# Kernel tuning notes

Measured on AMD Instinct MI355X. Metric: run time of the kernel, lower is better.

Reference implementation:

```python
import jax, jax.numpy as jnp
import numpy as np

B, T, N_EMBD, HEAD_SIZE = 4, 4096, 32, 32


def setup_inputs() -> dict:
    key = jax.random.key(0)
    k1, k2, k3, k4 = jax.random.split(key, 4)
    x = jax.random.normal(k1, (B, T, N_EMBD), dtype=jnp.float32)
    Wq = jax.random.normal(k2, (HEAD_SIZE, N_EMBD), dtype=jnp.float32) * (N_EMBD ** -0.5)
    Wk = jax.random.normal(k3, (HEAD_SIZE, N_EMBD), dtype=jnp.float32) * (N_EMBD ** -0.5)
    Wv = jax.random.normal(k4, (HEAD_SIZE, N_EMBD), dtype=jnp.float32) * (N_EMBD ** -0.5)
    return {"x": x, "Wq": Wq, "Wk": Wk, "Wv": Wv}


def reference(x, Wq, Wk, Wv):
    # Linear(bias=False): y = x @ W.T  -> [B, T, head_size]
    q = jnp.einsum('btn,hn->bth', x, Wq)
    k = jnp.einsum('btn,hn->bth', x, Wk)
    v = jnp.einsum('btn,hn->bth', x, Wv)
    scale = q.shape[-1] ** -0.5
    # [B, T, T] attention scores
    wei = jnp.einsum('bth,bsh->bts', q, k) * scale
    # Faithful to source: tril the scores, then mask entries equal to 0
    tril = jnp.tril(wei)
    wei = jax.nn.softmax(jnp.where(tril == 0, -jnp.inf, tril), axis=-1)
    return jnp.einsum('bts,bsh->bth', wei, v)
```

## Files before the change

### kernel.cpp

```cpp
#include <hip/hip_runtime.h>
#include <cmath>

#define BB 4
#define TT 4096
#define NE 32
#define HS 32

#define IPB 2176
#define MAXSP 16
#define SLOT 288
#define FNEG (-1.0e30f)
#define BIAS 6.0f

typedef unsigned int uint32;
typedef __fp16 half2v __attribute__((ext_vector_type(2)));
typedef __fp16 half4v __attribute__((ext_vector_type(4)));
typedef __fp16 half8v __attribute__((ext_vector_type(8)));
typedef float f32x4 __attribute__((ext_vector_type(4)));

__device__ __forceinline__ half2v u2h(uint32 u) {
    union { uint32 u; half2v h; } x; x.u = u; return x.h;
}

#if __has_builtin(__builtin_amdgcn_cvt_pkrtz)
__device__ __forceinline__ half2v pkf16(float a, float b) {
    return __builtin_amdgcn_cvt_pkrtz(a, b);
}
#else
__device__ __forceinline__ half2v pkf16(float a, float b) {
    half2v h; h.x = (__fp16)a; h.y = (__fp16)b; return h;
}
#endif

__global__ __launch_bounds__(256) void qkv_proj(
    const float* __restrict__ x,
    const float* __restrict__ Wq,
    const float* __restrict__ Wk,
    const float* __restrict__ Wv,
    __fp16* __restrict__ Qh, __fp16* __restrict__ Kh,
    __fp16* __restrict__ Vt4)
{
    int tid = blockIdx.x * 256 + threadIdx.x;
    int row = tid >> 5;
    int h   = tid & 31;
    const float4* xr4 = reinterpret_cast<const float4*>(x + (size_t)row * NE);
    float4 xv4[8];
    #pragma unroll
    for (int k = 0; k < 8; ++k) xv4[k] = xr4[k];
    const float* xv = (const float*)xv4;
    float aq = 0.f, ak = 0.f, av = 0.f;
    #pragma unroll
    for (int d = 0; d < NE; ++d) {
        aq = fmaf(xv[d], Wq[h * NE + d], aq);
        ak = fmaf(xv[d], Wk[h * NE + d], ak);
        av = fmaf(xv[d], Wv[h * NE + d], av);
    }
    size_t o = (size_t)row * HS + h;
    Qh[o] = (__fp16)aq;
    Kh[o] = (__fp16)ak;
    int b = row >> 12, t = row & (TT - 1);
    Vt4[((size_t)(b * (TT / 4) + (t >> 2)) * HS + h) * 4 + (t & 3)] = (__fp16)av;
}

__global__ __launch_bounds__(256, 6) void attn_partial(
    const __fp16* __restrict__ Qh, const __fp16* __restrict__ Kh,
    const __fp16* __restrict__ Vt4, float* __restrict__ part)
{
    const float SC2 = 0.17677669529663687f * 1.4426950408889634f;

    int wave = threadIdx.x >> 6;
    int lane = threadIdx.x & 63;
    int item = blockIdx.x * 4 + wave;
    int b = item / IPB;
    int r = item - b * IPB;
    int g = (int)((sqrtf((float)(4 + 2 * r)) - 2.0f) * 0.25f);
    if (g < 0) g = 0;
    while (8 * (g + 1) * (g + 2) <= r) ++g;
    while (8 * g * (g + 1) > r) --g;
    int rr = r - 8 * g * (g + 1);
    int tq = rr / (g + 1);
    int t  = 16 * g + tq;
    int sp = rr - tq * (g + 1);
    int qt0 = t * 16;
    int kbase = sp * 256;
    int kend  = min(kbase + 256, qt0 + 16);
    int nsub  = (kend - kbase) >> 4;

    int c = lane & 15;
    int q = lane >> 4;

    const __fp16* Qb = Qh  + (size_t)b * TT * HS;
    const __fp16* Kb = Kh  + (size_t)b * TT * HS;
    const __fp16* Vb = Vt4 + (size_t)b * (TT / 4) * HS * 4;

    union U4H8 { uint4 u; half8v h; };
    union U2H4 { uint2 u; half4v h; };
    union H4   { half4v h4; half2v h2[2]; };
    union H2U2 { half2v h[2]; uint2 u; };

    U4H8 qf; qf.u = *(const uint4*)(Qb + (size_t)(qt0 + c) * HS + 8 * q);

    const f32x4 zero = {0.f, 0.f, 0.f, 0.f};
    float l0 = 0.f, l1 = 0.f;
    f32x4 oa0 = zero, oa1 = zero, ob0 = zero, ob1 = zero;

    auto do16 = [&](int kb, float& l, f32x4& o0, f32x4& o1) {
        U4H8 kf; kf.u = *(const uint4*)(Kb + (size_t)(kb + c) * HS + 8 * q);
        const __fp16* vrow = Vb + (size_t)((kb >> 2) + q) * (HS * 4);
        U2H4 vf0; vf0.u = *(const uint2*)(vrow + c * 4);
        U2H4 vf1; vf1.u = *(const uint2*)(vrow + (c + 16) * 4);
        f32x4 s = __builtin_amdgcn_mfma_f32_16x16x32_f16(kf.h, qf.h, zero, 0, 0, 0);
        bool diag = (kb == qt0);
        float w[4];
        #pragma unroll
        for (int j = 0; j < 4; ++j) {
            w[j] = (s[j] != 0.0f) ? s[j] * SC2 : FNEG;
            if (diag && (4 * q + j > c)) w[j] = FNEG;
        }
        float p0 = exp2f(w[0] - BIAS), p1 = exp2f(w[1] - BIAS);
        float p2 = exp2f(w[2] - BIAS), p3 = exp2f(w[3] - BIAS);
        l += (p0 + p1) + (p2 + p3);
        H4 pf; pf.h2[0] = pkf16(p0, p1); pf.h2[1] = pkf16(p2, p3);
        o0 = __builtin_amdgcn_mfma_f32_16x16x16f16(vf0.h, pf.h4, o0, 0, 0, 0);
        o1 = __builtin_amdgcn_mfma_f32_16x16x16f16(vf1.h, pf.h4, o1, 0, 0, 0);
    };

    if (nsub == 16) {
        #pragma unroll 2
        for (int i = 0; i < 8; ++i) {
            do16(kbase + 32 * i,      l0, oa0, oa1);
            do16(kbase + 32 * i + 16, l1, ob0, ob1);
        }
    } else {
        int i = 0;
        for (; i + 1 < nsub; i += 2) {
            do16(kbase + 16 * i,      l0, oa0, oa1);
            do16(kbase + 16 * i + 16, l1, ob0, ob1);
        }
        if (i < nsub) do16(kbase + 16 * i, l0, oa0, oa1);
    }

    float l = l0 + l1;
    f32x4 o0, o1;
    #pragma unroll
    for (int k = 0; k < 4; ++k) {
        o0[k] = oa0[k] + ob0[k];
        o1[k] = oa1[k] + ob1[k];
    }

    float lt = l + __shfl_xor(l, 16);
    lt += __shfl_xor(lt, 32);

    float* P = part + (size_t)((b * 256 + t) * MAXSP + sp) * SLOT;
    if (q == 0) P[16 + c] = lt;
    uint32* Od = (uint32*)(P + 32) + c * 16 + 2 * q;
    H2U2 a;
    a.h[0] = pkf16(o0[0], o0[1]); a.h[1] = pkf16(o0[2], o0[3]);
    *(uint2*)Od = a.u;
    a.h[0] = pkf16(o1[0], o1[1]); a.h[1] = pkf16(o1[2], o1[3]);
    *(uint2*)(Od + 8) = a.u;
}

__global__ __launch_bounds__(256) void attn_combine(
    const float* __restrict__ part, float* __restrict__ out)
{
    int tid = blockIdx.x * 256 + threadIdx.x;
    int hq = tid & 3;
    int c  = (tid >> 2) & 15;
    int t  = (tid >> 6) & 255;
    int b  = tid >> 14;
    int ns = (t >> 4) + 1;

    const float* base = part + (size_t)(b * 256 + t) * MAXSP * SLOT;

    float acc[8];
    #pragma unroll
    for (int k = 0; k < 8; ++k) acc[k] = 0.f;
    float L = 0.f;
    for (int s = 0; s < ns; ++s) {
        const float* P = base + (size_t)s * SLOT;
        L += P[16 + c];
        uint4 ov = *(const uint4*)((const uint32*)(P + 32) + c * 16 + 4 * hq);
        const uint32* ovp = (const uint32*)&ov;
        #pragma unroll
        for (int pr = 0; pr < 4; ++pr) {
            half2v hh = u2h(ovp[pr]);
            acc[2 * pr]     += (float)hh.x;
            acc[2 * pr + 1] += (float)hh.y;
        }
    }
    float invL = 1.0f / L;
    float* orow = out + ((size_t)(b * TT + t * 16 + c)) * HS + 8 * hq;
    float4 o0 = {acc[0] * invL, acc[1] * invL, acc[2] * invL, acc[3] * invL};
    float4 o1 = {acc[4] * invL, acc[5] * invL, acc[6] * invL, acc[7] * invL};
    *(float4*)orow = o0;
    *(float4*)(orow + 4) = o1;
}

extern "C" void kernel_launch(void* const* d_in, const int* in_sizes, int n_in,
                              void* d_out, int out_size, void* d_ws, size_t ws_size,
                              hipStream_t stream)
{
    const float* x  = (const float*)d_in[0];
    const float* Wq = (const float*)d_in[1];
    const float* Wk = (const float*)d_in[2];
    const float* Wv = (const float*)d_in[3];
    float* out = (float*)d_out;

    __fp16* Qh  = (__fp16*)d_ws;
    __fp16* Kh  = Qh + (size_t)BB * TT * HS;
    __fp16* Vt4 = Kh + (size_t)BB * TT * HS;
    float* part = (float*)(Vt4 + (size_t)BB * TT * HS);

    qkv_proj<<<dim3((BB * TT * HS) / 256), dim3(256), 0, stream>>>(
        x, Wq, Wk, Wv, Qh, Kh, Vt4);
    attn_partial<<<dim3((BB * IPB) / 4), dim3(256), 0, stream>>>(
        Qh, Kh, Vt4, part);
    attn_combine<<<dim3(256), dim3(256), 0, stream>>>(part, out);
}
```

Before: 115.6 us.

## Fold softmax scale into Q, bias into MFMA accumulator, interleave V layout

Pre-scales Q by the softmax scale times log2(e) in the projection kernel, and seeds the QK MFMA accumulator with -BIAS. This removes the per-element multiply and subtract in the inner loop. V is re-laid out so each lane fetches both head halves in one 16-byte load instead of two 8-byte loads, and the partial output is stored with a single 16-byte store; the combine kernel's output indexing is adjusted to match. Scaling Q before the fp16 cast changes rounding, and the zero test now compares against -BIAS, which slightly alters the semantics of masking scores that are exactly zero.

```diff
diff --git a/kernel.cpp b/kernel.cpp
--- a/kernel.cpp
+++ b/kernel.cpp
@@ -11,6 +11,7 @@
 #define SLOT 288
 #define FNEG (-1.0e30f)
 #define BIAS 6.0f
+#define SC2  0.25506953149031156f
 
 typedef unsigned int uint32;
 typedef __fp16 half2v __attribute__((ext_vector_type(2)));
@@ -38,7 +39,7 @@
     const float* __restrict__ Wk,
     const float* __restrict__ Wv,
     __fp16* __restrict__ Qh, __fp16* __restrict__ Kh,
-    __fp16* __restrict__ Vt4)
+    __fp16* __restrict__ Vt8)
 {
     int tid = blockIdx.x * 256 + threadIdx.x;
     int row = tid >> 5;
@@ -56,18 +57,17 @@
         av = fmaf(xv[d], Wv[h * NE + d], av);
     }
     size_t o = (size_t)row * HS + h;
-    Qh[o] = (__fp16)aq;
+    Qh[o] = (__fp16)(aq * SC2);
     Kh[o] = (__fp16)ak;
     int b = row >> 12, t = row & (TT - 1);
-    Vt4[((size_t)(b * (TT / 4) + (t >> 2)) * HS + h) * 4 + (t & 3)] = (__fp16)av;
+    Vt8[((size_t)(b * (TT / 4) + (t >> 2)) * 16 + (h & 15)) * 8
+        + (h >> 4) * 4 + (t & 3)] = (__fp16)av;
 }
 
 __global__ __launch_bounds__(256, 6) void attn_partial(
     const __fp16* __restrict__ Qh, const __fp16* __restrict__ Kh,
-    const __fp16* __restrict__ Vt4, float* __restrict__ part)
-{
-    const float SC2 = 0.17677669529663687f * 1.4426950408889634f;
-
+    const __fp16* __restrict__ Vt8, float* __restrict__ part)
+{
     int wave = threadIdx.x >> 6;
     int lane = threadIdx.x & 63;
     int item = blockIdx.x * 4 + wave;
@@ -91,38 +91,36 @@
 
     const __fp16* Qb = Qh  + (size_t)b * TT * HS;
     const __fp16* Kb = Kh  + (size_t)b * TT * HS;
-    const __fp16* Vb = Vt4 + (size_t)b * (TT / 4) * HS * 4;
-
-    union U4H8 { uint4 u; half8v h; };
-    union U2H4 { uint2 u; half4v h; };
-    union H4   { half4v h4; half2v h2[2]; };
-    union H2U2 { half2v h[2]; uint2 u; };
+    const __fp16* Vb = Vt8 + (size_t)b * (TT / 4) * 128;
+
+    union U4H8  { uint4 u; half8v h; };
+    union U4H44 { uint4 u; half4v h4[2]; };
+    union H4    { half4v h4; half2v h2[2]; };
+    union H4U4  { half2v h[4]; uint4 u; };
 
     U4H8 qf; qf.u = *(const uint4*)(Qb + (size_t)(qt0 + c) * HS + 8 * q);
 
-    const f32x4 zero = {0.f, 0.f, 0.f, 0.f};
+    const f32x4 cbias = {-BIAS, -BIAS, -BIAS, -BIAS};
     float l0 = 0.f, l1 = 0.f;
-    f32x4 oa0 = zero, oa1 = zero, ob0 = zero, ob1 = zero;
+    f32x4 oa0 = {0.f,0.f,0.f,0.f}, oa1 = oa0, ob0 = oa0, ob1 = oa0;
 
     auto do16 = [&](int kb, float& l, f32x4& o0, f32x4& o1) {
         U4H8 kf; kf.u = *(const uint4*)(Kb + (size_t)(kb + c) * HS + 8 * q);
-        const __fp16* vrow = Vb + (size_t)((kb >> 2) + q) * (HS * 4);
-        U2H4 vf0; vf0.u = *(const uint2*)(vrow + c * 4);
-        U2H4 vf1; vf1.u = *(const uint2*)(vrow + (c + 16) * 4);
-        f32x4 s = __builtin_amdgcn_mfma_f32_16x16x32_f16(kf.h, qf.h, zero, 0, 0, 0);
+        U4H44 vf; vf.u = *(const uint4*)(Vb + (size_t)((kb >> 2) + q) * 128 + c * 8);
+        f32x4 s = __builtin_amdgcn_mfma_f32_16x16x32_f16(kf.h, qf.h, cbias, 0, 0, 0);
         bool diag = (kb == qt0);
         float w[4];
         #pragma unroll
         for (int j = 0; j < 4; ++j) {
-            w[j] = (s[j] != 0.0f) ? s[j] * SC2 : FNEG;
+            w[j] = (s[j] != -BIAS) ? s[j] : FNEG;
             if (diag && (4 * q + j > c)) w[j] = FNEG;
         }
-        float p0 = exp2f(w[0] - BIAS), p1 = exp2f(w[1] - BIAS);
-        float p2 = exp2f(w[2] - BIAS), p3 = exp2f(w[3] - BIAS);
+        float p0 = exp2f(w[0]), p1 = exp2f(w[1]);
+        float p2 = exp2f(w[2]), p3 = exp2f(w[3]);
         l += (p0 + p1) + (p2 + p3);
         H4 pf; pf.h2[0] = pkf16(p0, p1); pf.h2[1] = pkf16(p2, p3);
-        o0 = __builtin_amdgcn_mfma_f32_16x16x16f16(vf0.h, pf.h4, o0, 0, 0, 0);
-        o1 = __builtin_amdgcn_mfma_f32_16x16x16f16(vf1.h, pf.h4, o1, 0, 0, 0);
+        o0 = __builtin_amdgcn_mfma_f32_16x16x16f16(vf.h4[0], pf.h4, o0, 0, 0, 0);
+        o1 = __builtin_amdgcn_mfma_f32_16x16x16f16(vf.h4[1], pf.h4, o1, 0, 0, 0);
     };
 
     if (nsub == 16) {
@@ -153,12 +151,10 @@
 
     float* P = part + (size_t)((b * 256 + t) * MAXSP + sp) * SLOT;
     if (q == 0) P[16 + c] = lt;
-    uint32* Od = (uint32*)(P + 32) + c * 16 + 2 * q;
-    H2U2 a;
+    H4U4 a;
     a.h[0] = pkf16(o0[0], o0[1]); a.h[1] = pkf16(o0[2], o0[3]);
-    *(uint2*)Od = a.u;
-    a.h[0] = pkf16(o1[0], o1[1]); a.h[1] = pkf16(o1[2], o1[3]);
-    *(uint2*)(Od + 8) = a.u;
+    a.h[2] = pkf16(o1[0], o1[1]); a.h[3] = pkf16(o1[2], o1[3]);
+    *((uint4*)((uint32*)(P + 32) + c * 16 + q * 4)) = a.u;
 }
 
 __global__ __launch_bounds__(256) void attn_combine(
@@ -190,11 +186,11 @@
         }
     }
     float invL = 1.0f / L;
-    float* orow = out + ((size_t)(b * TT + t * 16 + c)) * HS + 8 * hq;
-    float4 o0 = {acc[0] * invL, acc[1] * invL, acc[2] * invL, acc[3] * invL};
-    float4 o1 = {acc[4] * invL, acc[5] * invL, acc[6] * invL, acc[7] * invL};
-    *(float4*)orow = o0;
-    *(float4*)(orow + 4) = o1;
+    float* orow = out + ((size_t)(b * TT + t * 16 + c)) * HS;
+    float4 w0 = {acc[0] * invL, acc[1] * invL, acc[2] * invL, acc[3] * invL};
+    float4 w1 = {acc[4] * invL, acc[5] * invL, acc[6] * invL, acc[7] * invL};
+    *(float4*)(orow + 4 * hq) = w0;
+    *(float4*)(orow + 16 + 4 * hq) = w1;
 }
 
 extern "C" void kernel_launch(void* const* d_in, const int* in_sizes, int n_in,
@@ -209,12 +205,12 @@
 
     __fp16* Qh  = (__fp16*)d_ws;
     __fp16* Kh  = Qh + (size_t)BB * TT * HS;
-    __fp16* Vt4 = Kh + (size_t)BB * TT * HS;
-    float* part = (float*)(Vt4 + (size_t)BB * TT * HS);
+    __fp16* Vt8 = Kh + (size_t)BB * TT * HS;
+    float* part = (float*)(Vt8 + (size_t)BB * TT * HS);
 
     qkv_proj<<<dim3((BB * TT * HS) / 256), dim3(256), 0, stream>>>(
-        x, Wq, Wk, Wv, Qh, Kh, Vt4);
+        x, Wq, Wk, Wv, Qh, Kh, Vt8);
     attn_partial<<<dim3((BB * IPB) / 4), dim3(256), 0, stream>>>(
-        Qh, Kh, Vt4, part);
+        Qh, Kh, Vt8, part);
     attn_combine<<<dim3(256), dim3(256), 0, stream>>>(part, out);
 }
```

Result: no change. 114.0 us (-1.4%).
